# Kernel tuning notes

Hardware: AMD Instinct MI355X
Metric: run time of the kernel (lower is better)

Reference implementation:

```python
import jax, jax.numpy as jnp
import numpy as np

B, L, D = 32, 512, 256
MAX_DUR = 8


def setup_inputs() -> dict:
    key = jax.random.key(0)
    k1, k2 = jax.random.split(key)
    hidden_phonems = jax.random.normal(k1, (B, L, D), dtype=jnp.float32)
    durations = jax.random.randint(k2, (B, L), 0, MAX_DUR, dtype=jnp.int32)
    return {"hidden_phonems": hidden_phonems, "durations": durations}


def reference(hidden_phonems, durations):
    # hidden_phonems: [B, L, D], durations: [B, L] int
    totals = jnp.sum(durations, axis=1)                    # [B] mel length per utterance
    max_T = int(jnp.max(totals))                           # batch-max padded length (matches torch)
    cum = jnp.cumsum(durations, axis=1)                    # [B, L] exclusive-of-next prefix sums
    t = jnp.arange(max_T, dtype=jnp.int32)                 # output frame positions
    # frame t belongs to the first phoneme whose cumulative duration exceeds t
    idx = jax.vmap(lambda c: jnp.searchsorted(c, t, side='right'))(cum)  # [B, max_T]
    idx = jnp.clip(idx, 0, hidden_phonems.shape[1] - 1)
    out = jnp.take_along_axis(hidden_phonems, idx[:, :, None], axis=1)   # [B, max_T, D]
    mask = (t[None, :] < totals[:, None])                  # zero out padding frames
    return out * mask[:, :, None].astype(out.dtype)
```

## Files before the change

### kernel.cpp

```cpp
#include <hip/hip_runtime.h>
#include <hip/hip_bf16.h>

#define B_SZ 32
#define L_SZ 512
#define D_SZ 256

__global__ void scan_kernel(const int* __restrict__ durations,
                            int* __restrict__ cum) {
    __shared__ int s[L_SZ];
    const int b = blockIdx.x;
    const int tid = threadIdx.x;

    s[tid] = durations[b * L_SZ + tid];
    __syncthreads();

    #pragma unroll
    for (int off = 1; off < L_SZ; off <<= 1) {
        int v = (tid >= off) ? s[tid - off] : 0;
        __syncthreads();
        s[tid] += v;
        __syncthreads();
    }

    cum[b * L_SZ + tid] = s[tid];
}

__global__ void __launch_bounds__(256)
fill_kernel(const float* __restrict__ hidden,
            const int* __restrict__ cum,
            float* __restrict__ out,
            int maxT, int tiles_per_b) {
    __shared__ int scum[L_SZ];
    const int b = blockIdx.x / tiles_per_b;
    const int tile = blockIdx.x % tiles_per_b;
    const int tid = threadIdx.x;

    scum[tid]        = cum[b * L_SZ + tid];
    scum[tid + 256]  = cum[b * L_SZ + tid + 256];
    __syncthreads();

    const int total = scum[L_SZ - 1];
    const int wave = tid >> 6;
    const int lane = tid & 63;
    const int t = tile * 4 + wave;
    if (t >= maxT) return;

    float4 val = make_float4(0.f, 0.f, 0.f, 0.f);
    if (t < total) {
        int lo = 0, hi = L_SZ - 1;
        while (lo < hi) {
            int mid = (lo + hi) >> 1;
            if (scum[mid] <= t) lo = mid + 1; else hi = mid;
        }
        const float4* src =
            (const float4*)(hidden + ((size_t)b * L_SZ + lo) * D_SZ);
        val = src[lane];
    }
    float4* dst = (float4*)(out + ((size_t)b * maxT + t) * D_SZ);
    dst[lane] = val;
}

extern "C" void kernel_launch(void* const* d_in, const int* in_sizes, int n_in,
                              void* d_out, int out_size, void* d_ws, size_t ws_size,
                              hipStream_t stream) {
    const float* hidden = (const float*)d_in[0];
    const int* durations = (const int*)d_in[1];
    float* out = (float*)d_out;

    int* cum = (int*)d_ws;

    const int maxT = out_size / (B_SZ * D_SZ);
    const int tiles_per_b = (maxT + 3) / 4;

    scan_kernel<<<B_SZ, L_SZ, 0, stream>>>(durations, cum);
    fill_kernel<<<B_SZ * tiles_per_b, 256, 0, stream>>>(hidden, cum, out,
                                                        maxT, tiles_per_b);
}
```

Baseline: 89.02 us.

## Replace per-frame binary search with per-phoneme scatter expansion

Instead of one wave per output frame doing a binary search over cumulative durations, each wave now handles one phoneme, loads its row once and writes it to all of its duration frames. Separate blocks zero-fill padding frames past each utterance's total. This removes the search and the repeated gather reads. In exchange it relies on durations being at most 7 and makes the work per wave uneven.

```diff
diff --git a/kernel.cpp b/kernel.cpp
--- a/kernel.cpp
+++ b/kernel.cpp
@@ -4,6 +4,8 @@
 #define B_SZ 32
 #define L_SZ 512
 #define D_SZ 256
+#define PHON_BLOCKS (B_SZ * L_SZ / 4)
+#define PAD_FRAMES_PER_BLOCK 16
 
 __global__ void scan_kernel(const int* __restrict__ durations,
                             int* __restrict__ cum) {
@@ -26,38 +28,52 @@
 }
 
 __global__ void __launch_bounds__(256)
-fill_kernel(const float* __restrict__ hidden,
-            const int* __restrict__ cum,
-            float* __restrict__ out,
-            int maxT, int tiles_per_b) {
-    __shared__ int scum[L_SZ];
-    const int b = blockIdx.x / tiles_per_b;
-    const int tile = blockIdx.x % tiles_per_b;
-    const int tid = threadIdx.x;
+expand_kernel(const float* __restrict__ hidden,
+              const int* __restrict__ durations,
+              const int* __restrict__ cum,
+              float* __restrict__ out,
+              int maxT, int padBlocksPerB) {
+    const int tid  = threadIdx.x;
+    const int lane = tid & 63;
+    const int wave = tid >> 6;
 
-    scum[tid]        = cum[b * L_SZ + tid];
-    scum[tid + 256]  = cum[b * L_SZ + tid + 256];
-    __syncthreads();
+    if (blockIdx.x < PHON_BLOCKS) {
+        const int wid = blockIdx.x * 4 + wave;
+        const int b = wid >> 9;
+        const int l = wid & (L_SZ - 1);
+        const int d = durations[b * L_SZ + l];
+        if (d == 0) return;
+        const int end   = cum[b * L_SZ + l];
+        const int start = end - d;
 
-    const int total = scum[L_SZ - 1];
-    const int wave = tid >> 6;
-    const int lane = tid & 63;
-    const int t = tile * 4 + wave;
-    if (t >= maxT) return;
+        const float4* src =
+            (const float4*)(hidden + ((size_t)(b * L_SZ + l)) * D_SZ);
+        float4 v = src[lane];
 
-    float4 val = make_float4(0.f, 0.f, 0.f, 0.f);
-    if (t < total) {
-        int lo = 0, hi = L_SZ - 1;
-        while (lo < hi) {
-            int mid = (lo + hi) >> 1;
-            if (scum[mid] <= t) lo = mid + 1; else hi = mid;
+        float4* dst =
+            (float4*)(out + ((size_t)b * maxT + start) * D_SZ) + lane;
+        #pragma unroll
+        for (int j = 0; j < 7; ++j) {
+            if (j < d) dst[j * 64] = v;
         }
-        const float4* src =
-            (const float4*)(hidden + ((size_t)b * L_SZ + lo) * D_SZ);
-        val = src[lane];
+    } else {
+        const int pb   = blockIdx.x - PHON_BLOCKS;
+        const int b    = pb / padBlocksPerB;
+        const int tile = pb % padBlocksPerB;
+        const int total = cum[b * L_SZ + (L_SZ - 1)];
+        const int t0 = tile * PAD_FRAMES_PER_BLOCK;
+        if (t0 + PAD_FRAMES_PER_BLOCK <= total) return;
+
+        const float4 z = make_float4(0.f, 0.f, 0.f, 0.f);
+        #pragma unroll
+        for (int i = 0; i < 4; ++i) {
+            const int t = t0 + wave * 4 + i;
+            if (t >= total && t < maxT) {
+                float4* dst = (float4*)(out + ((size_t)b * maxT + t) * D_SZ);
+                dst[lane] = z;
+            }
+        }
     }
-    float4* dst = (float4*)(out + ((size_t)b * maxT + t) * D_SZ);
-    dst[lane] = val;
 }
 
 extern "C" void kernel_launch(void* const* d_in, const int* in_sizes, int n_in,
@@ -70,9 +86,10 @@
     int* cum = (int*)d_ws;
 
     const int maxT = out_size / (B_SZ * D_SZ);
-    const int tiles_per_b = (maxT + 3) / 4;
+    const int padBlocksPerB = (maxT + PAD_FRAMES_PER_BLOCK - 1) / PAD_FRAMES_PER_BLOCK;
+    const int grid = PHON_BLOCKS + B_SZ * padBlocksPerB;
 
     scan_kernel<<<B_SZ, L_SZ, 0, stream>>>(durations, cum);
-    fill_kernel<<<B_SZ * tiles_per_b, 256, 0, stream>>>(hidden, cum, out,
-                                                        maxT, tiles_per_b);
+    expand_kernel<<<grid, 256, 0, stream>>>(hidden, durations, cum, out,
+                                            maxT, padBlocksPerB);
 }
```

Result: faster. 84.61 us (-5.0%).
